# Kernel optimization log

Hardware: AMD Instinct MI355X
Metric: run time of the kernel (lower is better)

Reference implementation:

```python
import jax, jax.numpy as jnp
import numpy as np

N = 50000        # num nodes
E = 800000       # num edges (before self loops)
IN = 256         # in_channels
H = 4            # heads
C = 32           # out_channels per head
NEG_SLOPE = 0.2


def _glorot(key, shape):
    fan = shape[-2] * (shape[-1] if len(shape) > 2 else 1) + shape[-1]
    # PyG glorot: uniform(-s, s) with s = sqrt(6 / (fan_in + fan_out))
    s = float(np.sqrt(6.0 / (shape[-2] + shape[-1])))
    return jax.random.uniform(key, shape, jnp.float32, -s, s)


def setup_inputs() -> dict:
    key = jax.random.key(0)
    k1, k2, k3, k4, k5 = jax.random.split(key, 5)
    x = jax.random.normal(k1, (N, IN), jnp.float32)
    src = jax.random.randint(k2, (E,), 0, N)
    dst = jax.random.randint(k3, (E,), 0, N)
    # guarantee no self loops (module removes them then re-adds exactly N loops)
    dst = jnp.where(dst == src, (dst + 1) % N, dst)
    edge_index = jnp.stack([src, dst]).astype(jnp.int32)
    weight = _glorot(k4, (IN, H * C))
    att = _glorot(k5, (1, H, 2 * C))
    bias = jnp.zeros((H * C,), jnp.float32)
    return {"x": x, "weight": weight, "att": att, "bias": bias,
            "edge_index": edge_index}


def reference(x, weight, att, bias, edge_index):
    n = x.shape[0]
    # linear projection -> [N, H, C]
    h = (x @ weight).reshape(n, H, C)
    # add self loops (input edge_index has none)
    loops = jnp.arange(n, dtype=edge_index.dtype)
    ei = jnp.concatenate([edge_index, jnp.stack([loops, loops])], axis=1)
    src, dst = ei[0], ei[1]          # flow source_to_target: j=src(row 0), i=dst(row 1)
    x_j = h[src]                     # [E', H, C] source features
    x_i = h[dst]                     # [E', H, C] target features
    wl = att[:, :, :C]               # applied to x_i (first half of concat)
    wr = att[:, :, C:]               # applied to x_j
    alpha = (x_i * wl).sum(-1) + (x_j * wr).sum(-1)   # [E', H]
    alpha = jax.nn.leaky_relu(alpha, NEG_SLOPE)
    # NOTE: module normalizes softmax over edge_index[0] (src) segments
    seg = src
    amax = jax.ops.segment_max(alpha, seg, num_segments=n)
    alpha = jnp.exp(alpha - amax[seg])
    denom = jax.ops.segment_sum(alpha, seg, num_segments=n)
    alpha = alpha / (denom[seg] + 1e-16)
    # weighted messages, aggregated at edge_index[i] = edge_index[1] (dst)
    msg = x_j * alpha[:, :, None]                     # [E', H, C]
    out = jax.ops.segment_sum(msg, dst, num_segments=n)  # [N, H, C]
    return out.reshape(n, H * C) + bias
```

## Files before the change

### kernel.cpp

```cpp
#include <hip/hip_runtime.h>
#include <hip/hip_fp16.h>
#include <math.h>


#define NH 4
#define CH 32
#define HC 128
#define IND 256
#define NEG_SLOPE 0.2f
#define CSH 8
#define NCB_MAX 256
#define CHUNK 4096
#define BCAP 6144

typedef __attribute__((ext_vector_type(8))) short bf16x8;
typedef __attribute__((ext_vector_type(16))) float f32x16;

__device__ __forceinline__ unsigned short f2bf(float f) {
    unsigned int u = __float_as_uint(f);
    unsigned int r = (u + 0x7FFFu + ((u >> 16) & 1u)) >> 16;
    return (unsigned short)r;
}
__device__ __forceinline__ float bf2f(unsigned short s) {
    return __uint_as_float(((unsigned int)s) << 16);
}

__global__ __launch_bounds__(256) void k_wprep(const float* __restrict__ W,
                                               unsigned short* __restrict__ WT_bf,
                                               int* __restrict__ gcurS,
                                               int* __restrict__ gcurD) {
    int t = blockIdx.x * 256 + threadIdx.x;
    if (blockIdx.x == 0) { gcurS[threadIdx.x] = 0; gcurD[threadIdx.x] = 0; }
    if (t < IND * HC) {
        int c = t >> 8;
        int k = t & 255;
        WT_bf[t] = f2bf(W[k * HC + c]);
    }
}

__global__ __launch_bounds__(256) void k_gs(const float* __restrict__ x,
                                            const unsigned short* __restrict__ WT_bf,
                                            const float* __restrict__ att,
                                            unsigned short* __restrict__ h_bf,
                                            float* __restrict__ al,
                                            float* __restrict__ ar,
                                            const int* __restrict__ ei,
                                            int* __restrict__ gcurS,
                                            int* __restrict__ gcurD,
                                            unsigned int* __restrict__ recS,
                                            unsigned int* __restrict__ recD,
                                            int E, int NE, int ncb, int nsb, int N) {
    __shared__ float cs[128 * 129];

    const int tid = threadIdx.x;

    if (blockIdx.x < nsb) {
        unsigned int* srt = (unsigned int*)cs;
        int* cntS  = (int*)(srt + CHUNK);
        int* cntD  = cntS + 256;
        int* offS  = cntD + 256;
        int* offD  = offS + 256;
        int* curSl = offD + 256;
        int* curDl = curSl + 256;
        int* gposS = curDl + 256;
        int* gposD = gposS + 256;
        int* wsumS = gposD + 256;
        int* wsumD = wsumS + 4;

        const int lane = tid & 63;
        const int wv   = tid >> 6;
        const int t0   = blockIdx.x * CHUNK;
        const int m    = min(CHUNK, NE - t0);

        cntS[tid] = 0; cntD[tid] = 0;

        unsigned int myrec[16];
        unsigned int mval = 0;
#pragma unroll
        for (int j = 0; j < 16; j++) {
            int i = j * 256 + tid;
            int t = t0 + i;
            int src = 0, dst = 0;
            if (i < m) {
                mval |= 1u << j;
                if (t < E) { src = ei[t]; dst = ei[E + t]; }
                else       { src = dst = t - E; }
            }
            myrec[j] = (unsigned int)src | ((unsigned int)dst << 16);
        }
        __syncthreads();

#pragma unroll
        for (int j = 0; j < 16; j++) {
            if (mval & (1u << j)) {
                unsigned int r = myrec[j];
                atomicAdd(&cntS[(r & 0xFFFFu) >> CSH], 1);
                atomicAdd(&cntD[(r >> 16) >> CSH], 1);
            }
        }
        __syncthreads();

        int vS = cntS[tid], vD = cntD[tid];
        int sS = vS, sD = vD;
#pragma unroll
        for (int d = 1; d < 64; d <<= 1) {
            int tS = __shfl_up(sS, d, 64);
            int tD = __shfl_up(sD, d, 64);
            if (lane >= d) { sS += tS; sD += tD; }
        }
        if (lane == 63) { wsumS[wv] = sS; wsumD[wv] = sD; }
        __syncthreads();
        int baseS = 0, baseD = 0;
        for (int w = 0; w < wv; w++) { baseS += wsumS[w]; baseD += wsumD[w]; }
        int exS = baseS + sS - vS;
        int exD = baseD + sD - vD;
        offS[tid] = exS; curSl[tid] = exS;
        offD[tid] = exD; curDl[tid] = exD;
        if (tid < ncb) {
            gposS[tid] = vS ? atomicAdd(&gcurS[tid], vS) : 0;
            gposD[tid] = vD ? atomicAdd(&gcurD[tid], vD) : 0;
        }
        __syncthreads();

#pragma unroll
        for (int j = 0; j < 16; j++) {
            if (mval & (1u << j)) {
                unsigned int r = myrec[j];
                int p = atomicAdd(&curSl[(r & 0xFFFFu) >> CSH], 1);
                srt[p] = r;
            }
        }
        __syncthreads();
        for (int i = tid; i < m; i += 256) {
            unsigned int r = srt[i];
            int cb = (int)(r & 0xFFFFu) >> CSH;
            int p  = gposS[cb] + (i - offS[cb]);
            if (p < BCAP)
                recS[(size_t)cb * BCAP + p] = r;
        }
        __syncthreads();

#pragma unroll
        for (int j = 0; j < 16; j++) {
            if (mval & (1u << j)) {
                unsigned int r = myrec[j];
                int p = atomicAdd(&curDl[(r >> 16) >> CSH], 1);
                srt[p] = r;
            }
        }
        __syncthreads();
        for (int i = tid; i < m; i += 256) {
            unsigned int r = srt[i];
            int cb = (int)(r >> 16) >> CSH;
            int p  = gposD[cb] + (i - offD[cb]);
            if (p < BCAP)
                recD[(size_t)cb * BCAP + p] = r;
        }
        return;
    }

    unsigned short* wsT = (unsigned short*)cs;

    const int row0 = (blockIdx.x - nsb) * 128;
    const int wave = tid >> 6;
    const int lane = tid & 63;
    const int n32  = lane & 31;
    const int half = lane >> 5;

    {
        int c  = tid >> 1;
        int kh = (tid & 1) * 128;
        const unsigned short* src = WT_bf + c * IND + kh;
        unsigned short* dst = wsT + c * 258 + kh;
#pragma unroll
        for (int j = 0; j < 128; j += 8)
            *(int4*)(dst + j) = *(const int4*)(src + j);
    }
    __syncthreads();

    const int row   = row0 + wave * 32 + n32;
    const bool valid = row < N;
    const float* xrow = x + (size_t)row * IND + half * 8;

    f32x16 acc[4];
#pragma unroll
    for (int t = 0; t < 4; t++)
#pragma unroll
        for (int r = 0; r < 16; r++) acc[t][r] = 0.0f;

#pragma unroll 4
    for (int s = 0; s < 16; s++) {
        float4 v0 = make_float4(0.f, 0.f, 0.f, 0.f);
        float4 v1 = v0;
        if (valid) {
            v0 = *(const float4*)(xrow + s * 16);
            v1 = *(const float4*)(xrow + s * 16 + 4);
        }
        bf16x8 a;
        a[0] = (short)f2bf(v0.x); a[1] = (short)f2bf(v0.y);
        a[2] = (short)f2bf(v0.z); a[3] = (short)f2bf(v0.w);
        a[4] = (short)f2bf(v1.x); a[5] = (short)f2bf(v1.y);
        a[6] = (short)f2bf(v1.z); a[7] = (short)f2bf(v1.w);
#pragma unroll
        for (int t = 0; t < 4; t++) {
            bf16x8 b = *(const bf16x8*)(wsT + (t * 32 + n32) * 258 + s * 16 + half * 8);
            acc[t] = __builtin_amdgcn_mfma_f32_32x32x16_bf16(a, b, acc[t], 0, 0, 0);
        }
    }
    __syncthreads();

#pragma unroll
    for (int t = 0; t < 4; t++)
#pragma unroll
        for (int r = 0; r < 16; r++) {
            int rl = wave * 32 + (r & 3) + 8 * (r >> 2) + 4 * half;
            cs[rl * 129 + t * 32 + n32] = acc[t][r];
        }
    __syncthreads();

    const int rl   = tid >> 1;
    const int chf  = tid & 1;
    const int orow = row0 + rl;
    if (orow < N) {
        const float* cr = cs + rl * 129 + chf * 64;
        unsigned short* hp = h_bf + (size_t)orow * HC + chf * 64;
#pragma unroll
        for (int c = 0; c < 64; c += 8) {
            ushort4 o0, o1;
            o0.x = f2bf(cr[c]);     o0.y = f2bf(cr[c + 1]);
            o0.z = f2bf(cr[c + 2]); o0.w = f2bf(cr[c + 3]);
            o1.x = f2bf(cr[c + 4]); o1.y = f2bf(cr[c + 5]);
            o1.z = f2bf(cr[c + 6]); o1.w = f2bf(cr[c + 7]);
            *(ushort4*)(hp + c) = o0;
            *(ushort4*)(hp + c + 4) = o1;
        }
        const int h0 = 2 * chf, h1 = 2 * chf + 1;
        const float* w0 = att + h0 * (2 * CH);
        const float* w1 = att + h1 * (2 * CH);
        float sl0 = 0.f, sr0 = 0.f, sl1 = 0.f, sr1 = 0.f;
#pragma unroll
        for (int c = 0; c < CH; c++) {
            float v0 = cr[c];
            float v1 = cr[CH + c];
            sl0 += v0 * w0[c];  sr0 += v0 * w0[CH + c];
            sl1 += v1 * w1[c];  sr1 += v1 * w1[CH + c];
        }
        al[orow * NH + h0] = sl0;  al[orow * NH + h1] = sl1;
        ar[orow * NH + h0] = sr0;  ar[orow * NH + h1] = sr1;
    }
}

__global__ __launch_bounds__(256) void k_bucket(const unsigned int* __restrict__ recS,
                                                const unsigned int* __restrict__ recD,
                                                const int* __restrict__ gcurS,
                                                const int* __restrict__ gcurD,
                                                const float* __restrict__ al,
                                                const float* __restrict__ ar,
                                                unsigned short* __restrict__ adjD,
                                                int* __restrict__ rowB,
                                                int* __restrict__ rowE,
                                                float* __restrict__ arw,
                                                int ncb, int N) {
    __shared__ int cnt[256], cur[256], sc[256];
    __shared__ float lsums[256 * NH];
    __shared__ float lar[256 * NH];
    const int tid = threadIdx.x;

    if (blockIdx.x < ncb) {
        const int cb = blockIdx.x;
        const int b0 = cb * BCAP;
        const int tot_rec = min(gcurD[cb], BCAP);

        cnt[tid] = 0;
        __syncthreads();
        for (int i = tid; i < tot_rec; i += 256) {
            unsigned int r = recD[b0 + i];
            atomicAdd(&cnt[(r >> 16) & 255], 1);
        }
        __syncthreads();
        int v = cnt[tid];
        sc[tid] = v;
        __syncthreads();
        for (int o = 1; o < 256; o <<= 1) {
            int t = (tid >= o) ? sc[tid - o] : 0;
            __syncthreads();
            sc[tid] += t;
            __syncthreads();
        }
        int ex = sc[tid] - v;
        int node_g = (cb << CSH) + tid;
        if (node_g < N) { rowB[node_g] = b0 + ex; rowE[node_g] = b0 + ex + v; }
        cur[tid] = ex;
        __syncthreads();
        for (int i = tid; i < tot_rec; i += 256) {
            unsigned int r = recD[b0 + i];
            int node = (int)(r >> 16) & 255;
            int p = atomicAdd(&cur[node], 1);
            adjD[b0 + p] = (unsigned short)(r & 0xFFFFu);
        }
    } else {
        const int cb = blockIdx.x - ncb;
        const int b0 = cb * BCAP;
        const int b1 = b0 + min(gcurS[cb], BCAP);
        const int node_g = (cb << CSH) + tid;

        float4 arv = make_float4(0.f, 0.f, 0.f, 0.f);
        if (node_g < N) arv = *(const float4*)(ar + (size_t)node_g * NH);
        *(float4*)(lar + tid * NH) = arv;
        *(float4*)(lsums + tid * NH) = make_float4(0.f, 0.f, 0.f, 0.f);
        __syncthreads();

        int i = b0 + tid;
        for (; i + 256 < b1; i += 512) {
            unsigned int r0 = recS[i];
            unsigned int r1 = recS[i + 256];
            int sl0 = (int)(r0 & 255u), dst0 = (int)(r0 >> 16);
            int sl1 = (int)(r1 & 255u), dst1 = (int)(r1 >> 16);
            float4 av0 = *(const float4*)(al + (size_t)dst0 * NH);
            float4 av1 = *(const float4*)(al + (size_t)dst1 * NH);
            const float* w0 = lar + sl0 * NH;
            const float* w1 = lar + sl1 * NH;
            float a0 = av0.x + w0[0], a1 = av0.y + w0[1];
            float a2 = av0.z + w0[2], a3 = av0.w + w0[3];
            float c0 = av1.x + w1[0], c1 = av1.y + w1[1];
            float c2 = av1.z + w1[2], c3 = av1.w + w1[3];
            a0 = (a0 > 0.f) ? a0 : NEG_SLOPE * a0;
            a1 = (a1 > 0.f) ? a1 : NEG_SLOPE * a1;
            a2 = (a2 > 0.f) ? a2 : NEG_SLOPE * a2;
            a3 = (a3 > 0.f) ? a3 : NEG_SLOPE * a3;
            c0 = (c0 > 0.f) ? c0 : NEG_SLOPE * c0;
            c1 = (c1 > 0.f) ? c1 : NEG_SLOPE * c1;
            c2 = (c2 > 0.f) ? c2 : NEG_SLOPE * c2;
            c3 = (c3 > 0.f) ? c3 : NEG_SLOPE * c3;
            float* s0 = lsums + sl0 * NH;
            float* s1 = lsums + sl1 * NH;
            atomicAdd(s0 + 0, __expf(a0));
            atomicAdd(s0 + 1, __expf(a1));
            atomicAdd(s0 + 2, __expf(a2));
            atomicAdd(s0 + 3, __expf(a3));
            atomicAdd(s1 + 0, __expf(c0));
            atomicAdd(s1 + 1, __expf(c1));
            atomicAdd(s1 + 2, __expf(c2));
            atomicAdd(s1 + 3, __expf(c3));
        }
        if (i < b1) {
            unsigned int r = recS[i];
            int slot = (int)(r & 255u);
            int dst  = (int)(r >> 16);
            float4 alv = *(const float4*)(al + (size_t)dst * NH);
            const float* av = lar + slot * NH;
            float a0 = alv.x + av[0], a1 = alv.y + av[1];
            float a2 = alv.z + av[2], a3 = alv.w + av[3];
            a0 = (a0 > 0.f) ? a0 : NEG_SLOPE * a0;
            a1 = (a1 > 0.f) ? a1 : NEG_SLOPE * a1;
            a2 = (a2 > 0.f) ? a2 : NEG_SLOPE * a2;
            a3 = (a3 > 0.f) ? a3 : NEG_SLOPE * a3;
            float* sp = lsums + slot * NH;
            atomicAdd(sp + 0, __expf(a0));
            atomicAdd(sp + 1, __expf(a1));
            atomicAdd(sp + 2, __expf(a2));
            atomicAdd(sp + 3, __expf(a3));
        }
        __syncthreads();

        if (node_g < N) {
            const float* sp = lsums + tid * NH;
            float4 p0 = make_float4(arv.x, 1.0f / (sp[0] + 1e-16f),
                                    arv.y, 1.0f / (sp[1] + 1e-16f));
            float4 p1 = make_float4(arv.z, 1.0f / (sp[2] + 1e-16f),
                                    arv.w, 1.0f / (sp[3] + 1e-16f));
            *(float4*)(arw + (size_t)node_g * 8)     = p0;
            *(float4*)(arw + (size_t)node_g * 8 + 4) = p1;
        }
    }
}

__global__ __launch_bounds__(256) void k_agg(const int* __restrict__ rowB,
                                             const int* __restrict__ rowE,
                                             const unsigned short* __restrict__ adjD,
                                             const float* __restrict__ al,
                                             const float* __restrict__ arw,
                                             const unsigned short* __restrict__ h_bf,
                                             const float* __restrict__ bias,
                                             float* __restrict__ out, int N) {
    const int g = threadIdx.x >> 5;
    const int n = blockIdx.x * 8 + g;
    if (n >= N) return;
    const int l  = threadIdx.x & 31;
    const int c0 = l * 4;
    const int hh = l >> 3;
    const int beg = rowB[n], end = rowE[n];
    const float alv = al[n * NH + hh];

    float a0 = 0.f, a1 = 0.f, a2 = 0.f, a3 = 0.f;

    for (int base = beg; base < end; base += 32) {
        int idx = base + l;
        int av  = (idx < end) ? (int)adjD[idx] : 0;
        int cnt = min(32, end - base);
        int e = 0;
        for (; e + 4 <= cnt; e += 4) {
            int s0 = __shfl(av, e,     32);
            int s1 = __shfl(av, e + 1, 32);
            int s2 = __shfl(av, e + 2, 32);
            int s3 = __shfl(av, e + 3, 32);
            ushort4 u0 = *(const ushort4*)(h_bf + (size_t)s0 * HC + c0);
            ushort4 u1 = *(const ushort4*)(h_bf + (size_t)s1 * HC + c0);
            ushort4 u2 = *(const ushort4*)(h_bf + (size_t)s2 * HC + c0);
            ushort4 u3 = *(const ushort4*)(h_bf + (size_t)s3 * HC + c0);
            float2 p0 = *(const float2*)(arw + (size_t)s0 * 8 + hh * 2);
            float2 p1 = *(const float2*)(arw + (size_t)s1 * 8 + hh * 2);
            float2 p2 = *(const float2*)(arw + (size_t)s2 * 8 + hh * 2);
            float2 p3 = *(const float2*)(arw + (size_t)s3 * 8 + hh * 2);
            float t0 = alv + p0.x; t0 = (t0 > 0.f) ? t0 : NEG_SLOPE * t0;
            float t1 = alv + p1.x; t1 = (t1 > 0.f) ? t1 : NEG_SLOPE * t1;
            float t2 = alv + p2.x; t2 = (t2 > 0.f) ? t2 : NEG_SLOPE * t2;
            float t3 = alv + p3.x; t3 = (t3 > 0.f) ? t3 : NEG_SLOPE * t3;
            float w0 = __expf(t0) * p0.y;
            float w1 = __expf(t1) * p1.y;
            float w2 = __expf(t2) * p2.y;
            float w3 = __expf(t3) * p3.y;
            a0 += bf2f(u0.x) * w0; a1 += bf2f(u0.y) * w0;
            a2 += bf2f(u0.z) * w0; a3 += bf2f(u0.w) * w0;
            a0 += bf2f(u1.x) * w1; a1 += bf2f(u1.y) * w1;
            a2 += bf2f(u1.z) * w1; a3 += bf2f(u1.w) * w1;
            a0 += bf2f(u2.x) * w2; a1 += bf2f(u2.y) * w2;
            a2 += bf2f(u2.z) * w2; a3 += bf2f(u2.w) * w2;
            a0 += bf2f(u3.x) * w3; a1 += bf2f(u3.y) * w3;
            a2 += bf2f(u3.z) * w3; a3 += bf2f(u3.w) * w3;
        }
        for (; e < cnt; e++) {
            int s0 = __shfl(av, e, 32);
            ushort4 u0 = *(const ushort4*)(h_bf + (size_t)s0 * HC + c0);
            float2 p0 = *(const float2*)(arw + (size_t)s0 * 8 + hh * 2);
            float t0 = alv + p0.x; t0 = (t0 > 0.f) ? t0 : NEG_SLOPE * t0;
            float w0 = __expf(t0) * p0.y;
            a0 += bf2f(u0.x) * w0; a1 += bf2f(u0.y) * w0;
            a2 += bf2f(u0.z) * w0; a3 += bf2f(u0.w) * w0;
        }
    }
    float4 b4 = *(const float4*)(bias + c0);
    *(float4*)(out + (size_t)n * HC + c0) =
        make_float4(a0 + b4.x, a1 + b4.y, a2 + b4.z, a3 + b4.w);
}

extern "C" void kernel_launch(void* const* d_in, const int* in_sizes, int n_in,
                              void* d_out, int out_size, void* d_ws, size_t ws_size,
                              hipStream_t stream) {
    const float* x    = (const float*)d_in[0];
    const float* W    = (const float*)d_in[1];
    const float* att  = (const float*)d_in[2];
    const float* bias = (const float*)d_in[3];
    const int*   ei   = (const int*)d_in[4];

    const int N  = in_sizes[0] / IND;
    const int E  = in_sizes[4] / 2;
    const int NE = E + N;
    const int ncb = (N + (1 << CSH) - 1) >> CSH;
    const int nsb = (NE + CHUNK - 1) / CHUNK;
    const int ngb = (N + 127) / 128;
    float* out = (float*)d_out;
    const int nodeTot = N * NH;
    const size_t capTot = (size_t)ncb * BCAP;

    unsigned short* h_bf  = (unsigned short*)d_ws;
    unsigned short* WT_bf = h_bf + (size_t)N * HC;
    float* al   = (float*)(WT_bf + IND * HC);
    float* ar   = al + nodeTot;
    float* arw  = ar + nodeTot;
    unsigned int* recS = (unsigned int*)(arw + (size_t)N * 8);
    unsigned int* recD = recS + capTot;
    unsigned short* adjD = (unsigned short*)(recD + capTot);
    int* rowB    = (int*)(adjD + capTot + (capTot & 1));
    int* rowE    = rowB + N;
    int* gcurS   = rowE + N;
    int* gcurD   = gcurS + NCB_MAX;

    k_wprep<<<(IND * HC + 255) / 256, 256, 0, stream>>>(W, WT_bf, gcurS, gcurD);
    k_gs<<<nsb + ngb, 256, 0, stream>>>(x, WT_bf, att, h_bf, al, ar, ei,
                                        gcurS, gcurD, recS, recD,
                                        E, NE, ncb, nsb, N);
    k_bucket<<<2 * ncb, 256, 0, stream>>>(recS, recD, gcurS, gcurD, al, ar,
                                          adjD, rowB, rowE, arw, ncb, N);
    k_agg<<<(N + 7) / 8, 256, 0, stream>>>(rowB, rowE, adjD, al, arw, h_bf,
                                           bias, out, N);
}
```

Baseline: 197.6 us.

## Keep per-head weight slices in registers and shrink LDS footprint in projection

```diff
diff --git a/kernel.cpp b/kernel.cpp
--- a/kernel.cpp
+++ b/kernel.cpp
@@ -50,12 +50,12 @@
                                             unsigned int* __restrict__ recS,
                                             unsigned int* __restrict__ recD,
                                             int E, int NE, int ncb, int nsb, int N) {
-    __shared__ float cs[128 * 129];
+    __shared__ unsigned int smem[6152];
 
     const int tid = threadIdx.x;
 
     if (blockIdx.x < nsb) {
-        unsigned int* srt = (unsigned int*)cs;
+        unsigned int* srt = smem;
         int* cntS  = (int*)(srt + CHUNK);
         int* cntD  = cntS + 256;
         int* offS  = cntD + 256;
@@ -159,94 +159,105 @@
         return;
     }
 
-    unsigned short* wsT = (unsigned short*)cs;
-
     const int row0 = (blockIdx.x - nsb) * 128;
     const int wave = tid >> 6;
     const int lane = tid & 63;
     const int n32  = lane & 31;
     const int half = lane >> 5;
 
+    float* lt = (float*)smem + wave * (32 * 33);
+
+    bf16x8 b0, b1, b2, b3, b4, b5, b6, b7, b8, b9, b10, b11, b12, b13, b14, b15;
     {
-        int c  = tid >> 1;
-        int kh = (tid & 1) * 128;
-        const unsigned short* src = WT_bf + c * IND + kh;
-        unsigned short* dst = wsT + c * 258 + kh;
-#pragma unroll
-        for (int j = 0; j < 128; j += 8)
-            *(int4*)(dst + j) = *(const int4*)(src + j);
-    }
-    __syncthreads();
-
-    const int row   = row0 + wave * 32 + n32;
-    const bool valid = row < N;
-    const float* xrow = x + (size_t)row * IND + half * 8;
-
-    f32x16 acc[4];
-#pragma unroll
-    for (int t = 0; t < 4; t++)
-#pragma unroll
-        for (int r = 0; r < 16; r++) acc[t][r] = 0.0f;
-
-#pragma unroll 4
-    for (int s = 0; s < 16; s++) {
-        float4 v0 = make_float4(0.f, 0.f, 0.f, 0.f);
-        float4 v1 = v0;
-        if (valid) {
-            v0 = *(const float4*)(xrow + s * 16);
-            v1 = *(const float4*)(xrow + s * 16 + 4);
-        }
-        bf16x8 a;
-        a[0] = (short)f2bf(v0.x); a[1] = (short)f2bf(v0.y);
-        a[2] = (short)f2bf(v0.z); a[3] = (short)f2bf(v0.w);
-        a[4] = (short)f2bf(v1.x); a[5] = (short)f2bf(v1.y);
-        a[6] = (short)f2bf(v1.z); a[7] = (short)f2bf(v1.w);
-#pragma unroll
-        for (int t = 0; t < 4; t++) {
-            bf16x8 b = *(const bf16x8*)(wsT + (t * 32 + n32) * 258 + s * 16 + half * 8);
-            acc[t] = __builtin_amdgcn_mfma_f32_32x32x16_bf16(a, b, acc[t], 0, 0, 0);
-        }
-    }
-    __syncthreads();
-
-#pragma unroll
-    for (int t = 0; t < 4; t++)
+        const unsigned short* wp = WT_bf + (size_t)(wave * 32 + n32) * IND + half * 8;
+        b0  = *(const bf16x8*)(wp + 0 * 16);
+        b1  = *(const bf16x8*)(wp + 1 * 16);
+        b2  = *(const bf16x8*)(wp + 2 * 16);
+        b3  = *(const bf16x8*)(wp + 3 * 16);
+        b4  = *(const bf16x8*)(wp + 4 * 16);
+        b5  = *(const bf16x8*)(wp + 5 * 16);
+        b6  = *(const bf16x8*)(wp + 6 * 16);
+        b7  = *(const bf16x8*)(wp + 7 * 16);
+        b8  = *(const bf16x8*)(wp + 8 * 16);
+        b9  = *(const bf16x8*)(wp + 9 * 16);
+        b10 = *(const bf16x8*)(wp + 10 * 16);
+        b11 = *(const bf16x8*)(wp + 11 * 16);
+        b12 = *(const bf16x8*)(wp + 12 * 16);
+        b13 = *(const bf16x8*)(wp + 13 * 16);
+        b14 = *(const bf16x8*)(wp + 14 * 16);
+        b15 = *(const bf16x8*)(wp + 15 * 16);
+    }
+
+    const float* wl = att + wave * (2 * CH) + half * 16;
+
+    for (int t = 0; t < 4; t++) {
+        const int row   = row0 + t * 32 + n32;
+        const bool valid = row < N;
+        const float* xrow = x + (size_t)row * IND + half * 8;
+
+        f32x16 acc;
+#pragma unroll
+        for (int r = 0; r < 16; r++) acc[r] = 0.0f;
+
+#define KSTEP(s, bs)                                                         \
+        {                                                                    \
+            float4 v0 = make_float4(0.f, 0.f, 0.f, 0.f);                     \
+            float4 v1 = v0;                                                  \
+            if (valid) {                                                     \
+                v0 = *(const float4*)(xrow + (s) * 16);                      \
+                v1 = *(const float4*)(xrow + (s) * 16 + 4);                  \
+            }                                                                \
+            bf16x8 a;                                                        \
+            a[0] = (short)f2bf(v0.x); a[1] = (short)f2bf(v0.y);              \
+            a[2] = (short)f2bf(v0.z); a[3] = (short)f2bf(v0.w);              \
+            a[4] = (short)f2bf(v1.x); a[5] = (short)f2bf(v1.y);              \
+            a[6] = (short)f2bf(v1.z); a[7] = (short)f2bf(v1.w);              \
+            acc = __builtin_amdgcn_mfma_f32_32x32x16_bf16(a, bs, acc, 0, 0, 0); \
+        }
+        KSTEP(0, b0)   KSTEP(1, b1)   KSTEP(2, b2)   KSTEP(3, b3)
+        KSTEP(4, b4)   KSTEP(5, b5)   KSTEP(6, b6)   KSTEP(7, b7)
+        KSTEP(8, b8)   KSTEP(9, b9)   KSTEP(10, b10) KSTEP(11, b11)
+        KSTEP(12, b12) KSTEP(13, b13) KSTEP(14, b14) KSTEP(15, b15)
+#undef KSTEP
+
 #pragma unroll
         for (int r = 0; r < 16; r++) {
-            int rl = wave * 32 + (r & 3) + 8 * (r >> 2) + 4 * half;
-            cs[rl * 129 + t * 32 + n32] = acc[t][r];
-        }
-    __syncthreads();
-
-    const int rl   = tid >> 1;
-    const int chf  = tid & 1;
-    const int orow = row0 + rl;
-    if (orow < N) {
-        const float* cr = cs + rl * 129 + chf * 64;
-        unsigned short* hp = h_bf + (size_t)orow * HC + chf * 64;
-#pragma unroll
-        for (int c = 0; c < 64; c += 8) {
-            ushort4 o0, o1;
-            o0.x = f2bf(cr[c]);     o0.y = f2bf(cr[c + 1]);
-            o0.z = f2bf(cr[c + 2]); o0.w = f2bf(cr[c + 3]);
-            o1.x = f2bf(cr[c + 4]); o1.y = f2bf(cr[c + 5]);
-            o1.z = f2bf(cr[c + 6]); o1.w = f2bf(cr[c + 7]);
-            *(ushort4*)(hp + c) = o0;
-            *(ushort4*)(hp + c + 4) = o1;
-        }
-        const int h0 = 2 * chf, h1 = 2 * chf + 1;
-        const float* w0 = att + h0 * (2 * CH);
-        const float* w1 = att + h1 * (2 * CH);
-        float sl0 = 0.f, sr0 = 0.f, sl1 = 0.f, sr1 = 0.f;
-#pragma unroll
-        for (int c = 0; c < CH; c++) {
-            float v0 = cr[c];
-            float v1 = cr[CH + c];
-            sl0 += v0 * w0[c];  sr0 += v0 * w0[CH + c];
-            sl1 += v1 * w1[c];  sr1 += v1 * w1[CH + c];
-        }
-        al[orow * NH + h0] = sl0;  al[orow * NH + h1] = sl1;
-        ar[orow * NH + h0] = sr0;  ar[orow * NH + h1] = sr1;
+            int rl = (r & 3) + 8 * (r >> 2) + 4 * half;
+            lt[rl * 33 + n32] = acc[r];
+        }
+        __builtin_amdgcn_sched_barrier(0);
+
+        const int grow = row0 + t * 32 + n32;
+        if (grow < N) {
+            const float* lr = lt + n32 * 33 + half * 16;
+            unsigned short* hp = h_bf + (size_t)grow * HC + wave * CH + half * 16;
+            ushort4 o0, o1, o2, o3;
+            o0.x = f2bf(lr[0]);  o0.y = f2bf(lr[1]);
+            o0.z = f2bf(lr[2]);  o0.w = f2bf(lr[3]);
+            o1.x = f2bf(lr[4]);  o1.y = f2bf(lr[5]);
+            o1.z = f2bf(lr[6]);  o1.w = f2bf(lr[7]);
+            o2.x = f2bf(lr[8]);  o2.y = f2bf(lr[9]);
+            o2.z = f2bf(lr[10]); o2.w = f2bf(lr[11]);
+            o3.x = f2bf(lr[12]); o3.y = f2bf(lr[13]);
+            o3.z = f2bf(lr[14]); o3.w = f2bf(lr[15]);
+            *(ushort4*)(hp + 0)  = o0;
+            *(ushort4*)(hp + 4)  = o1;
+            *(ushort4*)(hp + 8)  = o2;
+            *(ushort4*)(hp + 12) = o3;
+
+            float sl = 0.f, sr = 0.f;
+#pragma unroll
+            for (int j = 0; j < 16; j++) {
+                float v = lr[j];
+                sl += v * wl[j];
+                sr += v * wl[32 + j];
+            }
+            sl += __shfl_xor(sl, 32);
+            sr += __shfl_xor(sr, 32);
+            if (half == 0) al[grow * NH + wave] = sl;
+            else           ar[grow * NH + wave] = sr;
+        }
+        __builtin_amdgcn_sched_barrier(0);
     }
 }
 
```

Result: slower. 212.3 us (+7.4%).
